# Optimization experiments

Hardware: AMD Instinct MI355X
Metric: run time of the kernel (lower is better)

## Reference

```python
import jax, jax.numpy as jnp
import numpy as np

BS, NS, NO, REL_DIM, MEM_DIM = 2, 48, 48, 512, 256
LN_EPS = 1e-6


def setup_inputs() -> dict:
    key = jax.random.key(0)
    ks = jax.random.split(key, 4)
    s_in = 1.0 / np.sqrt(REL_DIM)
    s_mem = 1.0 / np.sqrt(MEM_DIM)
    return {
        "rel_reprs": jax.random.normal(ks[0], (BS, NS, NO, REL_DIM), dtype=jnp.float32),
        "W1": jax.random.normal(ks[1], (REL_DIM, MEM_DIM), dtype=jnp.float32) * s_in,
        "b1": jnp.zeros((MEM_DIM,), dtype=jnp.float32),
        "W2": jax.random.normal(ks[2], (REL_DIM, MEM_DIM), dtype=jnp.float32) * s_in,
        "b2": jnp.zeros((MEM_DIM,), dtype=jnp.float32),
        "We": jax.random.normal(ks[3], (MEM_DIM, MEM_DIM), dtype=jnp.float32) * s_mem,
        "be": jnp.zeros((MEM_DIM,), dtype=jnp.float32),
        "gamma": jnp.ones((MEM_DIM,), dtype=jnp.float32),
        "beta": jnp.zeros((MEM_DIM,), dtype=jnp.float32),
    }


def reference(rel_reprs, W1, b1, W2, b2, We, be, gamma, beta):
    # factor_type='sib', factor_encoder='biaf' (factorize=True), eval mode (dropout=identity).
    # Original: ha[b,s,o1,o2,:] = rel_reprs[b,s,o1,:]; hb[b,s,o1,o2,:] = rel_reprs[b,s,o2,:]
    # proj then broadcast (identical math to broadcasting then proj, since linears act on last dim).
    p1 = rel_reprs @ W1 + b1  # [bs, ns, no, mem]
    p2 = rel_reprs @ W2 + b2  # [bs, ns, no, mem]
    prod = p1[:, :, :, None, :] * p2[:, :, None, :, :]  # [bs, ns, no, no, mem]
    h = prod @ We + be  # encoder linear
    # LayerNorm(mem_dim, eps=1e-6)
    mu = jnp.mean(h, axis=-1, keepdims=True)
    var = jnp.mean(jnp.square(h - mu), axis=-1, keepdims=True)
    out = (h - mu) * jax.lax.rsqrt(var + LN_EPS) * gamma + beta
    return out
```

## Files before the change

kernel.cpp:

```cpp
#include <hip/hip_runtime.h>

typedef unsigned short ushort_t;
typedef __attribute__((ext_vector_type(8))) short bf16x8;
typedef __attribute__((ext_vector_type(4))) float f32x4;

#define BS 2
#define NS 48
#define NO 48
#define RD 512
#define MD 256
#define M1 (BS*NS*NO)
#define LN_EPS 1e-6f

__device__ __forceinline__ short f2bf(float f) {
    union { float f; unsigned u; } v; v.f = f;
    unsigned u = v.u;
    return (short)((u + 0x7fffu + ((u >> 16) & 1u)) >> 16);
}
__device__ __forceinline__ short f2bf_fast(float f) {
    union { float f; unsigned u; } v; v.f = f;
    return (short)((v.u + 0x8000u) >> 16);
}

__global__ __launch_bounds__(512) void prep_kernel(
    const float* __restrict__ W1, const float* __restrict__ W2,
    const float* __restrict__ We,
    ushort_t* __restrict__ w1F, ushort_t* __restrict__ w2F,
    ushort_t* __restrict__ weF)
{
    __shared__ float tile[64][65];
    int b = blockIdx.x;
    const float* src; ushort_t* dst; int NKS, kT, nT;
    if (b < 32)      { src = W1; dst = w1F; NKS = 16; kT = b >> 2;        nT = b & 3; }
    else if (b < 64) { src = W2; dst = w2F; NKS = 16; kT = (b - 32) >> 2; nT = b & 3; }
    else             { src = We; dst = weF; NKS = 8;  kT = (b - 64) >> 2; nT = b & 3; }
    int R0 = kT * 64, C0 = nT * 64;
    int tid = threadIdx.x;
#pragma unroll
    for (int pass = 0; pass < 2; ++pass) {
        int kl = pass * 32 + (tid >> 4);
        int nl = (tid & 15) * 4;
        float4 v = *reinterpret_cast<const float4*>(src + (size_t)(R0 + kl) * MD + C0 + nl);
        tile[kl][nl + 0] = v.x; tile[kl][nl + 1] = v.y;
        tile[kl][nl + 2] = v.z; tile[kl][nl + 3] = v.w;
    }
    __syncthreads();
    int f = tid >> 6, lane = tid & 63, lr = lane & 15, lg = lane >> 4;
    int ntl = f >> 1, ksl = f & 1;
    int ntG = (C0 >> 4) + ntl, ksG = (R0 >> 5) + ksl;
    bf16x8 v;
#pragma unroll
    for (int e = 0; e < 8; ++e)
        v[e] = f2bf(tile[ksl * 32 + lg * 8 + e][ntl * 16 + lr]);
    *reinterpret_cast<bf16x8*>(dst + ((size_t)(ntG * NKS + ksG) * 64 + lane) * 8) = v;
}

__global__ __launch_bounds__(256) void stage1_kernel(
    const float* __restrict__ rel,
    const ushort_t* __restrict__ w1F, const ushort_t* __restrict__ w2F,
    const float* __restrict__ b1, const float* __restrict__ b2,
    float* __restrict__ p1, float* __restrict__ p2)
{
    __shared__ __align__(16) char ldsA[16 * RD * 2];
    int blk = blockIdx.x;
    int mt = blk >> 1, which = blk & 1;
    const ushort_t* wF = which ? w2F : w1F;
    const float* bias  = which ? b2 : b1;
    float* out         = which ? p2 : p1;
    int tid = threadIdx.x, wid = tid >> 6, lane = tid & 63;
    int lr = lane & 15, lg = lane >> 4;

#pragma unroll
    for (int it = 0; it < 8; ++it) {
        int rr = it * 2 + (tid >> 7);
        int c  = (tid & 127) * 4;
        float4 v = *reinterpret_cast<const float4*>(rel + (size_t)(mt * 16 + rr) * RD + c);
        short4 s;
        s.x = f2bf_fast(v.x); s.y = f2bf_fast(v.y);
        s.z = f2bf_fast(v.z); s.w = f2bf_fast(v.w);
        *reinterpret_cast<short4*>(ldsA + rr * (RD * 2) + ((c * 2) ^ ((rr & 7) << 4))) = s;
    }
    __syncthreads();

    int n0 = wid * 64;
    f32x4 acc[4] = {};
#pragma unroll
    for (int ks = 0; ks < 16; ++ks) {
        bf16x8 a = *reinterpret_cast<const bf16x8*>(
            ldsA + lr * (RD * 2) + ((ks * 64 + lg * 16) ^ ((lr & 7) << 4)));
#pragma unroll
        for (int nt = 0; nt < 4; ++nt) {
            int ntG = (n0 >> 4) + nt;
            bf16x8 bfr = *reinterpret_cast<const bf16x8*>(
                wF + ((size_t)(ntG * 16 + ks) * 64 + lane) * 8);
            acc[nt] = __builtin_amdgcn_mfma_f32_16x16x32_bf16(a, bfr, acc[nt], 0, 0, 0);
        }
    }
#pragma unroll
    for (int nt = 0; nt < 4; ++nt) {
        int col = n0 + nt * 16 + lr;
        float bv = bias[col];
#pragma unroll
        for (int r = 0; r < 4; ++r) {
            int orow = mt * 16 + lg * 4 + r;
            out[(size_t)orow * MD + col] = acc[nt][r] + bv;
        }
    }
}

__global__ __launch_bounds__(512, 6) void stage2_kernel(
    const float* __restrict__ p1, const float* __restrict__ p2,
    const ushort_t* __restrict__ weF,
    const float* __restrict__ be, const float* __restrict__ gamma,
    const float* __restrict__ beta, float* __restrict__ out)
{
    __shared__ __align__(16) char lds[49152];
    __shared__ float pS1[NO][8];
    __shared__ float pS2[NO][8];
    __shared__ float muS[NO];
    __shared__ float rsS[NO];

    int d    = blockIdx.x;
    int bid  = (d & 7) * 576 + (d >> 3);
    int grp  = (bid / NO) * NO;
    int tid  = threadIdx.x;
    int wid  = tid >> 6;
    int lane = tid & 63;
    int lr   = lane & 15;
    int lg   = lane >> 4;
    int m0w  = wid * 32;

    const float* p1r = p1 + (size_t)bid * MD;
#pragma unroll
    for (int i = 0; i < 6; ++i) {
        int r  = i * 8 + wid;
        int m0 = lane * 4;
        float4 x = *reinterpret_cast<const float4*>(p1r + m0);
        float4 y = *reinterpret_cast<const float4*>(p2 + (size_t)(grp + r) * MD + m0);
        short4 s;
        s.x = f2bf_fast(x.x * y.x); s.y = f2bf_fast(x.y * y.y);
        s.z = f2bf_fast(x.z * y.z); s.w = f2bf_fast(x.w * y.w);
        *reinterpret_cast<short4*>(lds + r * (MD * 2) + ((m0 * 2) ^ ((r & 7) << 4))) = s;
    }
    __syncthreads();

    f32x4 acc[2][3] = {};
#pragma unroll
    for (int ks = 0; ks < 8; ++ks) {
        bf16x8 b[3];
#pragma unroll
        for (int nt = 0; nt < 3; ++nt) {
            int r = nt * 16 + lr;
            b[nt] = *reinterpret_cast<const bf16x8*>(
                lds + r * (MD * 2) + ((ks * 64 + lg * 16) ^ ((r & 7) << 4)));
        }
#pragma unroll
        for (int mt = 0; mt < 2; ++mt) {
            int ntG = wid * 2 + mt;
            bf16x8 af = *reinterpret_cast<const bf16x8*>(
                weF + ((size_t)(ntG * 8 + ks) * 64 + lane) * 8);
#pragma unroll
            for (int nt = 0; nt < 3; ++nt)
                acc[mt][nt] = __builtin_amdgcn_mfma_f32_16x16x32_bf16(
                    af, b[nt], acc[mt][nt], 0, 0, 0);
        }
    }

#pragma unroll
    for (int mt = 0; mt < 2; ++mt) {
        float4 bev = *reinterpret_cast<const float4*>(be + m0w + mt * 16 + lg * 4);
#pragma unroll
        for (int nt = 0; nt < 3; ++nt) {
            acc[mt][nt][0] += bev.x; acc[mt][nt][1] += bev.y;
            acc[mt][nt][2] += bev.z; acc[mt][nt][3] += bev.w;
        }
    }

#pragma unroll
    for (int nt = 0; nt < 3; ++nt) {
        float s1 = 0.f, s2 = 0.f;
#pragma unroll
        for (int mt = 0; mt < 2; ++mt)
#pragma unroll
            for (int r = 0; r < 4; ++r) {
                float v = acc[mt][nt][r];
                s1 += v; s2 += v * v;
            }
        s1 += __shfl_xor(s1, 16); s2 += __shfl_xor(s2, 16);
        s1 += __shfl_xor(s1, 32); s2 += __shfl_xor(s2, 32);
        if (lane < 16) {
            pS1[nt * 16 + lane][wid] = s1;
            pS2[nt * 16 + lane][wid] = s2;
        }
    }
    __syncthreads();

    if (tid < NO) {
        f32x4 a0 = *reinterpret_cast<const f32x4*>(&pS1[tid][0]);
        f32x4 a1 = *reinterpret_cast<const f32x4*>(&pS1[tid][4]);
        f32x4 b0 = *reinterpret_cast<const f32x4*>(&pS2[tid][0]);
        f32x4 b1v = *reinterpret_cast<const f32x4*>(&pS2[tid][4]);
        float S1 = a0[0]+a0[1]+a0[2]+a0[3] + a1[0]+a1[1]+a1[2]+a1[3];
        float S2 = b0[0]+b0[1]+b0[2]+b0[3] + b1v[0]+b1v[1]+b1v[2]+b1v[3];
        float m  = S1 * (1.0f / MD);
        float var = S2 * (1.0f / MD) - m * m;
        muS[tid] = m;
        rsS[tid] = rsqrtf(var + LN_EPS);
    }
    __syncthreads();

    float4 g4[2], b4[2];
#pragma unroll
    for (int mt = 0; mt < 2; ++mt) {
        g4[mt] = *reinterpret_cast<const float4*>(gamma + m0w + mt * 16 + lg * 4);
        b4[mt] = *reinterpret_cast<const float4*>(beta  + m0w + mt * 16 + lg * 4);
    }
#pragma unroll
    for (int nt = 0; nt < 3; ++nt) {
        int r = nt * 16 + lr;
        float mu = muS[r];
        float rs = rsS[r];
#pragma unroll
        for (int mt = 0; mt < 2; ++mt) {
            float4 o;
            o.x = (acc[mt][nt][0] - mu) * rs * g4[mt].x + b4[mt].x;
            o.y = (acc[mt][nt][1] - mu) * rs * g4[mt].y + b4[mt].y;
            o.z = (acc[mt][nt][2] - mu) * rs * g4[mt].z + b4[mt].z;
            o.w = (acc[mt][nt][3] - mu) * rs * g4[mt].w + b4[mt].w;
            int n4 = (m0w + mt * 16 + lg * 4) * 4;
            *reinterpret_cast<float4*>(
                lds + nt * 16384 + lr * 1024 + (n4 ^ ((lr & 7) << 4))) = o;
        }
    }
    __syncthreads();

    size_t ob = (size_t)bid * NO * MD;
#pragma unroll
    for (int nt = 0; nt < 3; ++nt) {
#pragma unroll
        for (int j = 0; j < 2; ++j) {
            int rl = wid * 2 + j;
            float4 o = *reinterpret_cast<const float4*>(
                lds + nt * 16384 + rl * 1024 + ((lane * 16) ^ ((rl & 7) << 4)));
            *reinterpret_cast<float4*>(
                out + ob + (size_t)(nt * 16 + rl) * MD + lane * 4) = o;
        }
    }
}

extern "C" void kernel_launch(void* const* d_in, const int* in_sizes, int n_in,
                              void* d_out, int out_size, void* d_ws, size_t ws_size,
                              hipStream_t stream) {
    const float* rel   = (const float*)d_in[0];
    const float* W1    = (const float*)d_in[1];
    const float* b1    = (const float*)d_in[2];
    const float* W2    = (const float*)d_in[3];
    const float* b2    = (const float*)d_in[4];
    const float* We    = (const float*)d_in[5];
    const float* be    = (const float*)d_in[6];
    const float* gamma = (const float*)d_in[7];
    const float* beta  = (const float*)d_in[8];
    float* out = (float*)d_out;

    char* ws = (char*)d_ws;
    ushort_t* w1F = (ushort_t*)(ws);
    ushort_t* w2F = (ushort_t*)(ws + 524288);
    ushort_t* weF = (ushort_t*)(ws + 1048576);
    float*    p1  = (float*)   (ws + 1179648);
    float*    p2  = (float*)   (ws + 1179648 + 4718592);

    prep_kernel<<<80, 512, 0, stream>>>(W1, W2, We, w1F, w2F, weF);
    stage1_kernel<<<576, 256, 0, stream>>>(rel, w1F, w2F, b1, b2, p1, p2);
    stage2_kernel<<<M1, 512, 0, stream>>>(p1, p2, weF, be, gamma, beta, out);
}
```

Baseline: 87.48 us.

## Double stage2 block to 1024 threads, one 16-column tile per wave

Stage2 now runs 16 waves per block instead of 8, so each wave owns a single 16-wide output-column tile rather than two. The per-wave accumulator count halves, and the weight fragments are loaded in two groups of four. The first group is issued before the LDS barrier to overlap with the product staging. This raises wave-level parallelism and lowers register pressure. The cost is more barrier participants and a larger partial-sum reduction across 16 waves, and LDS per block is unchanged, so block residency may be limited.

```diff
diff --git a/kernel.cpp b/kernel.cpp
--- a/kernel.cpp
+++ b/kernel.cpp
@@ -108,15 +108,15 @@
     }
 }
 
-__global__ __launch_bounds__(512, 6) void stage2_kernel(
+__global__ __launch_bounds__(1024, 8) void stage2_kernel(
     const float* __restrict__ p1, const float* __restrict__ p2,
     const ushort_t* __restrict__ weF,
     const float* __restrict__ be, const float* __restrict__ gamma,
     const float* __restrict__ beta, float* __restrict__ out)
 {
     __shared__ __align__(16) char lds[49152];
-    __shared__ float pS1[NO][8];
-    __shared__ float pS2[NO][8];
+    __shared__ float pS1[NO][16];
+    __shared__ float pS2[NO][16];
     __shared__ float muS[NO];
     __shared__ float rsS[NO];
 
@@ -128,12 +128,12 @@
     int lane = tid & 63;
     int lr   = lane & 15;
     int lg   = lane >> 4;
-    int m0w  = wid * 32;
+    int m0w  = wid * 16;
 
     const float* p1r = p1 + (size_t)bid * MD;
 #pragma unroll
-    for (int i = 0; i < 6; ++i) {
-        int r  = i * 8 + wid;
+    for (int i = 0; i < 3; ++i) {
+        int r  = i * 16 + wid;
         int m0 = lane * 4;
         float4 x = *reinterpret_cast<const float4*>(p1r + m0);
         float4 y = *reinterpret_cast<const float4*>(p2 + (size_t)(grp + r) * MD + m0);
@@ -142,11 +142,17 @@
         s.z = f2bf_fast(x.z * y.z); s.w = f2bf_fast(x.w * y.w);
         *reinterpret_cast<short4*>(lds + r * (MD * 2) + ((m0 * 2) ^ ((r & 7) << 4))) = s;
     }
-    __syncthreads();
-
-    f32x4 acc[2][3] = {};
-#pragma unroll
-    for (int ks = 0; ks < 8; ++ks) {
+
+    bf16x8 af[4];
+#pragma unroll
+    for (int ks = 0; ks < 4; ++ks)
+        af[ks] = *reinterpret_cast<const bf16x8*>(
+            weF + ((size_t)(wid * 8 + ks) * 64 + lane) * 8);
+    __syncthreads();
+
+    f32x4 acc[3] = {};
+#pragma unroll
+    for (int ks = 0; ks < 4; ++ks) {
         bf16x8 b[3];
 #pragma unroll
         for (int nt = 0; nt < 3; ++nt) {
@@ -155,24 +161,36 @@
                 lds + r * (MD * 2) + ((ks * 64 + lg * 16) ^ ((r & 7) << 4)));
         }
 #pragma unroll
-        for (int mt = 0; mt < 2; ++mt) {
-            int ntG = wid * 2 + mt;
-            bf16x8 af = *reinterpret_cast<const bf16x8*>(
-                weF + ((size_t)(ntG * 8 + ks) * 64 + lane) * 8);
-#pragma unroll
-            for (int nt = 0; nt < 3; ++nt)
-                acc[mt][nt] = __builtin_amdgcn_mfma_f32_16x16x32_bf16(
-                    af, b[nt], acc[mt][nt], 0, 0, 0);
-        }
-    }
-
-#pragma unroll
-    for (int mt = 0; mt < 2; ++mt) {
-        float4 bev = *reinterpret_cast<const float4*>(be + m0w + mt * 16 + lg * 4);
+        for (int nt = 0; nt < 3; ++nt)
+            acc[nt] = __builtin_amdgcn_mfma_f32_16x16x32_bf16(
+                af[ks], b[nt], acc[nt], 0, 0, 0);
+    }
+
+#pragma unroll
+    for (int ks = 0; ks < 4; ++ks)
+        af[ks] = *reinterpret_cast<const bf16x8*>(
+            weF + ((size_t)(wid * 8 + ks + 4) * 64 + lane) * 8);
+#pragma unroll
+    for (int ks = 0; ks < 4; ++ks) {
+        bf16x8 b[3];
 #pragma unroll
         for (int nt = 0; nt < 3; ++nt) {
-            acc[mt][nt][0] += bev.x; acc[mt][nt][1] += bev.y;
-            acc[mt][nt][2] += bev.z; acc[mt][nt][3] += bev.w;
+            int r = nt * 16 + lr;
+            b[nt] = *reinterpret_cast<const bf16x8*>(
+                lds + r * (MD * 2) + (((ks + 4) * 64 + lg * 16) ^ ((r & 7) << 4)));
+        }
+#pragma unroll
+        for (int nt = 0; nt < 3; ++nt)
+            acc[nt] = __builtin_amdgcn_mfma_f32_16x16x32_bf16(
+                af[ks], b[nt], acc[nt], 0, 0, 0);
+    }
+
+    {
+        float4 bev = *reinterpret_cast<const float4*>(be + m0w + lg * 4);
+#pragma unroll
+        for (int nt = 0; nt < 3; ++nt) {
+            acc[nt][0] += bev.x; acc[nt][1] += bev.y;
+            acc[nt][2] += bev.z; acc[nt][3] += bev.w;
         }
     }
 
@@ -180,12 +198,10 @@
     for (int nt = 0; nt < 3; ++nt) {
         float s1 = 0.f, s2 = 0.f;
 #pragma unroll
-        for (int mt = 0; mt < 2; ++mt)
-#pragma unroll
-            for (int r = 0; r < 4; ++r) {
-                float v = acc[mt][nt][r];
-                s1 += v; s2 += v * v;
-            }
+        for (int r = 0; r < 4; ++r) {
+            float v = acc[nt][r];
+            s1 += v; s2 += v * v;
+        }
         s1 += __shfl_xor(s1, 16); s2 += __shfl_xor(s2, 16);
         s1 += __shfl_xor(s1, 32); s2 += __shfl_xor(s2, 32);
         if (lane < 16) {
@@ -196,12 +212,14 @@
     __syncthreads();
 
     if (tid < NO) {
-        f32x4 a0 = *reinterpret_cast<const f32x4*>(&pS1[tid][0]);
-        f32x4 a1 = *reinterpret_cast<const f32x4*>(&pS1[tid][4]);
-        f32x4 b0 = *reinterpret_cast<const f32x4*>(&pS2[tid][0]);
-        f32x4 b1v = *reinterpret_cast<const f32x4*>(&pS2[tid][4]);
-        float S1 = a0[0]+a0[1]+a0[2]+a0[3] + a1[0]+a1[1]+a1[2]+a1[3];
-        float S2 = b0[0]+b0[1]+b0[2]+b0[3] + b1v[0]+b1v[1]+b1v[2]+b1v[3];
+        float S1 = 0.f, S2 = 0.f;
+#pragma unroll
+        for (int w = 0; w < 4; ++w) {
+            f32x4 a = *reinterpret_cast<const f32x4*>(&pS1[tid][w * 4]);
+            f32x4 c = *reinterpret_cast<const f32x4*>(&pS2[tid][w * 4]);
+            S1 += a[0] + a[1] + a[2] + a[3];
+            S2 += c[0] + c[1] + c[2] + c[3];
+        }
         float m  = S1 * (1.0f / MD);
         float var = S2 * (1.0f / MD) - m * m;
         muS[tid] = m;
@@ -209,42 +227,32 @@
     }
     __syncthreads();
 
-    float4 g4[2], b4[2];
-#pragma unroll
-    for (int mt = 0; mt < 2; ++mt) {
-        g4[mt] = *reinterpret_cast<const float4*>(gamma + m0w + mt * 16 + lg * 4);
-        b4[mt] = *reinterpret_cast<const float4*>(beta  + m0w + mt * 16 + lg * 4);
-    }
+    float4 g4 = *reinterpret_cast<const float4*>(gamma + m0w + lg * 4);
+    float4 b4 = *reinterpret_cast<const float4*>(beta  + m0w + lg * 4);
 #pragma unroll
     for (int nt = 0; nt < 3; ++nt) {
         int r = nt * 16 + lr;
         float mu = muS[r];
         float rs = rsS[r];
-#pragma unroll
-        for (int mt = 0; mt < 2; ++mt) {
-            float4 o;
-            o.x = (acc[mt][nt][0] - mu) * rs * g4[mt].x + b4[mt].x;
-            o.y = (acc[mt][nt][1] - mu) * rs * g4[mt].y + b4[mt].y;
-            o.z = (acc[mt][nt][2] - mu) * rs * g4[mt].z + b4[mt].z;
-            o.w = (acc[mt][nt][3] - mu) * rs * g4[mt].w + b4[mt].w;
-            int n4 = (m0w + mt * 16 + lg * 4) * 4;
-            *reinterpret_cast<float4*>(
-                lds + nt * 16384 + lr * 1024 + (n4 ^ ((lr & 7) << 4))) = o;
-        }
+        float4 o;
+        o.x = (acc[nt][0] - mu) * rs * g4.x + b4.x;
+        o.y = (acc[nt][1] - mu) * rs * g4.y + b4.y;
+        o.z = (acc[nt][2] - mu) * rs * g4.z + b4.z;
+        o.w = (acc[nt][3] - mu) * rs * g4.w + b4.w;
+        int n4 = (m0w + lg * 4) * 4;
+        *reinterpret_cast<float4*>(
+            lds + nt * 16384 + lr * 1024 + (n4 ^ ((lr & 7) << 4))) = o;
     }
     __syncthreads();
 
     size_t ob = (size_t)bid * NO * MD;
 #pragma unroll
     for (int nt = 0; nt < 3; ++nt) {
-#pragma unroll
-        for (int j = 0; j < 2; ++j) {
-            int rl = wid * 2 + j;
-            float4 o = *reinterpret_cast<const float4*>(
-                lds + nt * 16384 + rl * 1024 + ((lane * 16) ^ ((rl & 7) << 4)));
-            *reinterpret_cast<float4*>(
-                out + ob + (size_t)(nt * 16 + rl) * MD + lane * 4) = o;
-        }
+        int rl = wid;
+        float4 o = *reinterpret_cast<const float4*>(
+            lds + nt * 16384 + rl * 1024 + ((lane * 16) ^ ((rl & 7) << 4)));
+        *reinterpret_cast<float4*>(
+            out + ob + (size_t)(nt * 16 + rl) * MD + lane * 4) = o;
     }
 }
 
@@ -271,5 +279,5 @@
 
     prep_kernel<<<80, 512, 0, stream>>>(W1, W2, We, w1F, w2F, weF);
     stage1_kernel<<<576, 256, 0, stream>>>(rel, w1F, w2F, b1, b2, p1, p2);
-    stage2_kernel<<<M1, 512, 0, stream>>>(p1, p2, weF, be, gamma, beta, out);
-}
+    stage2_kernel<<<M1, 1024, 0, stream>>>(p1, p2, weF, be, gamma, beta, out);
+}
```

Result: slower. 90.70 us (+3.7%).
